# Kernel optimization log

Measured on AMD Instinct MI355X. Metric: run time of the kernel, lower is better.

## Reference

```python
import jax, jax.numpy as jnp
import numpy as np

# Dimensions (see shape_source)
N, M, C = 64, 300, 768          # batch, tokens (=max_frames), token dim
LAMB, G, K = 2, 8, 64           # expansion, groups, clusters
GS = LAMB * C // G              # group_size = 192
DESC = K * GS                   # 12288 NeXtVLAD descriptor dim
NB, NCLS = 512, 701             # bottleneck, classes


def setup_inputs() -> dict:
    key = jax.random.key(0)
    ks = jax.random.split(key, 8)
    w = lambda i, shape: jax.random.normal(ks[i], shape, jnp.float32) * 0.02
    return {
        "features": jax.random.normal(ks[0], (N, M + 1, C), jnp.float32),
        # NeXtVLAD_block params
        "fc0_w": w(1, (LAMB * C, C)), "fc0_b": jnp.zeros((LAMB * C,), jnp.float32),
        "fcgk_w": w(2, (G * K, LAMB * C)), "fcgk_b": jnp.zeros((G * K,), jnp.float32),
        "fcg_w": w(3, (G, LAMB * C)), "fcg_b": jnp.zeros((G,), jnp.float32),
        "bn0_g": jnp.ones((M,), jnp.float32), "bn0_b": jnp.zeros((M,), jnp.float32),
        "cw2": jax.random.uniform(ks[4], (1, GS, K), jnp.float32),
        "bn1_g": jnp.ones((1,), jnp.float32), "bn1_b": jnp.zeros((1,), jnp.float32),
        # ClassBlock params (Linear -> BN -> Linear classifier)
        "cls_fc_w": w(5, (NB, DESC)), "cls_fc_b": jnp.zeros((NB,), jnp.float32),
        "cls_bn_g": jnp.ones((NB,), jnp.float32), "cls_bn_b": jnp.zeros((NB,), jnp.float32),
        "cls_w": w(6, (NCLS, NB)), "cls_b": jnp.zeros((NCLS,), jnp.float32),
    }


def reference(features, fc0_w, fc0_b, fcgk_w, fcgk_b, fcg_w, fcg_b,
              bn0_g, bn0_b, cw2, bn1_g, bn1_b,
              cls_fc_w, cls_fc_b, cls_bn_g, cls_bn_b, cls_w, cls_b):
    # Drop CLS token -> local descriptors (N, M, C). (transpose+vector2image
    # in the torch code is a pure rearrangement back to (N, M, C) tokens.)
    x = features[:, 1:]
    # 1) expand D -> lamb*D
    x_dot = jnp.einsum('nmc,ec->nme', x, fc0_w) + fc0_b           # (N, M, lamb*C)
    # 2) group: (N, M*G, group_size)
    x_tilde = x_dot.reshape(-1, M * G, GS)
    # 3) soft assignment logits, BN over the frame axis (inference-mode BN:
    #    running stats 0/1 -> pure per-frame affine), softmax over clusters
    WgkX = jnp.einsum('nme,fe->nmf', x_dot, fcgk_w) + fcgk_b      # (N, M, G*K)
    WgkX = WgkX * bn0_g[None, :, None] + bn0_b[None, :, None]
    alpha_gk = jax.nn.softmax(WgkX.reshape(-1, M * G, K), axis=-1)
    # 4) sigmoid group attention
    alpha_g = jax.nn.sigmoid(jnp.einsum('nme,ge->nmg', x_dot, fcg_w) + fcg_b)
    alpha_g = alpha_g.reshape(-1, M * G, 1)
    activation = alpha_gk * alpha_g                                # (N, M*G, K)
    # 5) aggregate residuals: vlad = act^T x_tilde - a_sum * centers
    a = jnp.sum(activation, axis=1, keepdims=True) * cw2           # (N, GS, K)
    vlad = jnp.einsum('npk,npd->ndk', activation, x_tilde) - a     # (N, GS, K)
    # 6) L1-normalize over group_size dim (F.normalize(vlad, 1): p=1, dim=1)
    norm = jnp.maximum(jnp.sum(jnp.abs(vlad), axis=1, keepdims=True), 1e-12)
    vlad = (vlad / norm).reshape(-1, DESC)
    # bn1 = BatchNorm1d(1), inference mode -> scalar affine
    vlad = vlad * bn1_g[0] + bn1_b[0]
    # ClassBlock: Linear -> BN (inference affine) -> classifier Linear
    f = jnp.einsum('nd,bd->nb', vlad, cls_fc_w) + cls_fc_b         # (N, NB)
    f = f * cls_bn_g + cls_bn_b
    cls = jnp.einsum('nb,cb->nc', f, cls_w) + cls_b                # (N, NCLS)
    return (cls, f)
```

## Files before the change

### kernel.cpp

```cpp
#include <hip/hip_runtime.h>
#include <hip/hip_bf16.h>

#define NN 64
#define MM 300
#define CC 768
#define EE 1536
#define GG 8
#define KK 64
#define FF 512
#define GS 192
#define PP 2400
#define DESC 12288
#define NMROWS 19200
#define NB 512
#define NCLS 701

typedef _Float16 v8h __attribute__((ext_vector_type(8)));
typedef _Float16 v4h __attribute__((ext_vector_type(4)));
typedef float    v4f __attribute__((ext_vector_type(4)));

#define GLOAD_LDS16(g, s) \
    __builtin_amdgcn_global_load_lds( \
        (const __attribute__((address_space(1))) void*)(g), \
        (__attribute__((address_space(3))) void*)(s), 16, 0, 0)

__global__ __launch_bounds__(256)
void setup_k(const float* __restrict__ features, const float* __restrict__ fc0_w,
             const float* __restrict__ fcgk_w, const float* __restrict__ fcg_w,
             const float* __restrict__ fc0_b, const float* __restrict__ fcgk_b,
             const float* __restrict__ fcg_b,
             _Float16* __restrict__ xf16, _Float16* __restrict__ w1f16,
             _Float16* __restrict__ w2f16, _Float16* __restrict__ w1t16,
             float* __restrict__ biasc, float* __restrict__ wgc)
{
    __shared__ __align__(16) char sm[16640];
    const int bid = blockIdx.x, tid = threadIdx.x;

    if (bid < 14400) {
        int idx = bid * 256 + tid;
        int row = idx / 192;
        int c4  = (idx - row * 192) * 4;
        int n = row / 300, m = row - n * 300;
        float4 v = *(const float4*)(features + ((size_t)(n * 301 + m + 1)) * CC + c4);
        v4h h = { (_Float16)v.x, (_Float16)v.y, (_Float16)v.z, (_Float16)v.w };
        *(v4h*)(xf16 + (size_t)row * CC + c4) = h;
        return;
    }
    if (bid < 15552) {
        int idx = (bid - 14400) * 256 + tid;
        float4 v = *(const float4*)(fc0_w + (size_t)idx * 4);
        v4h h = { (_Float16)v.x, (_Float16)v.y, (_Float16)v.z, (_Float16)v.w };
        *(v4h*)(w1f16 + (size_t)idx * 4) = h;
        return;
    }
    if (bid < 16320) {
        int idx = (bid - 15552) * 256 + tid;
        float4 v = *(const float4*)(fcgk_w + (size_t)idx * 4);
        v4h h = { (_Float16)v.x, (_Float16)v.y, (_Float16)v.z, (_Float16)v.w };
        *(v4h*)(w2f16 + (size_t)idx * 4) = h;
        return;
    }
    if (bid < 16608) {
        float (*T)[65] = (float(*)[65])sm;
        int b = bid - 16320;
        const int c0 = (b % 12) * 64, e0 = (b / 12) * 64;
        const int tc = tid & 63, te = tid >> 6;
        #pragma unroll
        for (int r = 0; r < 16; ++r) {
            int el = te * 16 + r;
            T[el][tc] = fc0_w[(size_t)(e0 + el) * CC + c0 + tc];
        }
        __syncthreads();
        #pragma unroll
        for (int r = 0; r < 16; ++r) {
            int cl = te * 16 + r;
            w1t16[(size_t)(c0 + cl) * EE + e0 + tc] = (_Float16)T[tc][cl];
        }
        return;
    }
    if (bid < 17128) {
        float* red = (float*)sm;
        int f = bid - 16608;
        const float* row = (f < FF) ? (fcgk_w + (size_t)f * EE)
                                    : (fcg_w + (size_t)(f - FF) * EE);
        float s = 0.f;
        for (int e = tid; e < EE; e += 256) s += row[e] * fc0_b[e];
        red[tid] = s;
        __syncthreads();
        for (int o = 128; o; o >>= 1) {
            if (tid < o) red[tid] += red[tid + o];
            __syncthreads();
        }
        if (tid == 0)
            biasc[f] = red[0] + ((f < FF) ? fcgk_b[f] : fcg_b[f - FF]);
        return;
    }
    {
        float (*red)[GG][64] = (float(*)[GG][64])sm;
        int b = bid - 17128;
        const int c = (b % 12) * 64 + (tid & 63);
        const int es = b / 12, q = tid >> 6;
        float acc[GG] = {};
        for (int e = es * 192 + q * 48; e < es * 192 + q * 48 + 48; ++e) {
            float w1v = fc0_w[(size_t)e * CC + c];
            #pragma unroll
            for (int g = 0; g < GG; ++g) acc[g] = fmaf(fcg_w[g * EE + e], w1v, acc[g]);
        }
        #pragma unroll
        for (int g = 0; g < GG; ++g) red[q][g][tid & 63] = acc[g];
        __syncthreads();
        if (tid < 64) {
            #pragma unroll
            for (int g = 0; g < GG; ++g) {
                float v = red[0][g][tid] + red[1][g][tid] + red[2][g][tid] + red[3][g][tid];
                atomicAdd(&wgc[g * CC + c], v);
            }
        }
        return;
    }
}

template<bool OUTF16, bool BN0, bool SOFTGATE, bool BIAS>
__global__ __launch_bounds__(256)
void hgemm_nt(const _Float16* __restrict__ A, const _Float16* __restrict__ B,
              const float* __restrict__ bias,
              const float* __restrict__ bn_g, const float* __restrict__ bn_b,
              const float* __restrict__ sig,
              void* __restrict__ Cout, int Ndim, int Kdim, int gx)
{
    __shared__ __align__(16) _Float16 As[128 * 32];
    __shared__ __align__(16) _Float16 Bs[128 * 32];

    const int tid  = threadIdx.x;
    const int bid  = blockIdx.x;
    const int wave = tid >> 6, lane = tid & 63;
    const int bx = bid % gx, by = bid / gx;
    const int wr = wave >> 1, wc = wave & 1;
    const int row0 = by * 128, col0 = bx * 128;

    const int r0 = tid >> 2, cs = tid & 3;
    const int cc = cs ^ ((r0 >> 1) & 3);
    const _Float16* ga0 = A + (size_t)(row0 + r0) * Kdim + cc * 8;
    const _Float16* ga1 = A + (size_t)(row0 + r0 + 64) * Kdim + cc * 8;
    const _Float16* gb0 = B + (size_t)(col0 + r0) * Kdim + cc * 8;
    const _Float16* gb1 = B + (size_t)(col0 + r0 + 64) * Kdim + cc * 8;
    _Float16* sa0 = As + wave * 512;
    _Float16* sa1 = As + 2048 + wave * 512;
    _Float16* sb0 = Bs + wave * 512;
    _Float16* sb1 = Bs + 2048 + wave * 512;

    v4f acc[4][4];
    #pragma unroll
    for (int i = 0; i < 4; ++i)
        #pragma unroll
        for (int j = 0; j < 4; ++j)
            acc[i][j] = (v4f){0.f, 0.f, 0.f, 0.f};

    const int fm = lane & 15, fq = lane >> 4;
    const int sw = (fm >> 1) & 3;
    const _Float16* arp = As + (wr * 64 + fm) * 32 + (fq ^ sw) * 8;
    const _Float16* brp = Bs + (wc * 64 + fm) * 32 + (fq ^ sw) * 8;

    for (int kt = 0; kt < Kdim; kt += 32) {
        GLOAD_LDS16(ga0 + kt, sa0);
        GLOAD_LDS16(ga1 + kt, sa1);
        GLOAD_LDS16(gb0 + kt, sb0);
        GLOAD_LDS16(gb1 + kt, sb1);
        __syncthreads();

        v8h af[4], bf[4];
        #pragma unroll
        for (int i = 0; i < 4; ++i) af[i] = *(const v8h*)(arp + i * 16 * 32);
        #pragma unroll
        for (int j = 0; j < 4; ++j) bf[j] = *(const v8h*)(brp + j * 16 * 32);
        #pragma unroll
        for (int i = 0; i < 4; ++i)
            #pragma unroll
            for (int j = 0; j < 4; ++j)
                acc[i][j] = __builtin_amdgcn_mfma_f32_16x16x32_f16(
                    af[i], bf[j], acc[i][j], 0, 0, 0);
        __syncthreads();
    }

    float bj[4];
    #pragma unroll
    for (int j = 0; j < 4; ++j)
        bj[j] = BIAS ? bias[col0 + wc * 64 + j * 16 + fm] : 0.f;

    if (SOFTGATE) {
        const int gidx = (col0 >> 6) + wc;
        #pragma unroll
        for (int i = 0; i < 4; ++i) {
            #pragma unroll
            for (int r = 0; r < 4; ++r) {
                int grow = row0 + wr * 64 + i * 16 + fq * 4 + r;
                int n = grow / 300, mm = grow - n * 300;
                float g = bn_g[mm], bb = bn_b[mm];
                float v[4];
                #pragma unroll
                for (int j = 0; j < 4; ++j)
                    v[j] = (acc[i][j][r] + bj[j]) * g + bb;
                float mx = fmaxf(fmaxf(v[0], v[1]), fmaxf(v[2], v[3]));
                #pragma unroll
                for (int w = 1; w < 16; w <<= 1) mx = fmaxf(mx, __shfl_xor(mx, w));
                float e[4], s = 0.f;
                #pragma unroll
                for (int j = 0; j < 4; ++j) { e[j] = __expf(v[j] - mx); s += e[j]; }
                #pragma unroll
                for (int w = 1; w < 16; w <<= 1) s += __shfl_xor(s, w);
                float gate = sig[(size_t)grow * GG + gidx];
                float inv = gate / s;
                _Float16* cp = (_Float16*)Cout + (size_t)grow * Ndim + col0 + wc * 64;
                #pragma unroll
                for (int j = 0; j < 4; ++j) cp[j * 16 + fm] = (_Float16)(e[j] * inv);
            }
        }
        return;
    }

    #pragma unroll
    for (int i = 0; i < 4; ++i) {
        #pragma unroll
        for (int r = 0; r < 4; ++r) {
            int grow = row0 + wr * 64 + i * 16 + fq * 4 + r;
            float g = 1.f, bb = 0.f;
            if (BN0) { int m = grow % 300; g = bn_g[m]; bb = bn_b[m]; }
            #pragma unroll
            for (int j = 0; j < 4; ++j) {
                int gcol = col0 + wc * 64 + j * 16 + fm;
                float v = acc[i][j][r] + bj[j];
                if (BN0) v = v * g + bb;
                if (OUTF16)
                    ((_Float16*)Cout)[(size_t)grow * Ndim + gcol] = (_Float16)v;
                else
                    ((float*)Cout)[(size_t)grow * Ndim + gcol] = v;
            }
        }
    }
}

__global__ __launch_bounds__(256)
void alpha_sig_k(const _Float16* __restrict__ x, const float* __restrict__ wgc,
                 const float* __restrict__ bgc, float* __restrict__ sig)
{
    __shared__ float W[GG * CC];
    for (int i = threadIdx.x; i < GG * CC; i += 256) W[i] = wgc[i];
    __syncthreads();

    const int wave = threadIdx.x >> 6;
    const int lane = threadIdx.x & 63;

    for (int rr = 0; rr < 4; ++rr) {
        int row = blockIdx.x * 16 + wave * 4 + rr;
        const _Float16* xr = x + (size_t)row * CC;
        float acc[GG] = {};
        for (int c = lane; c < CC; c += 64) {
            float xv = (float)xr[c];
            #pragma unroll
            for (int g = 0; g < GG; ++g) acc[g] = fmaf(xv, W[g * CC + c], acc[g]);
        }
        float myval = 0.f;
        #pragma unroll
        for (int g = 0; g < GG; ++g) {
            float s = acc[g];
            #pragma unroll
            for (int o = 32; o; o >>= 1) s += __shfl_xor(s, o);
            if (lane == g) myval = s + bgc[g];
        }
        if (lane < GG)
            sig[(size_t)row * GG + lane] = 1.f / (1.f + __expf(-myval));
    }
}

__global__ __launch_bounds__(256)
void vladact_k(const _Float16* __restrict__ act, const _Float16* __restrict__ xdot,
               float* __restrict__ part, float* __restrict__ apart)
{
    __shared__ __align__(16) char sm[8192];
    const int tid = threadIdx.x, bid = blockIdx.x;

    if (bid >= 1536) {
        float (*red)[64] = (float(*)[64])sm;
        int b = bid - 1536;
        const int ps = b & 7, n = b >> 3;
        const int k = tid & 63, q = tid >> 6;
        const _Float16* base = act + ((size_t)n * PP + ps * 300 + q * 75) * 64 + k;
        float s = 0.f;
        for (int p = 0; p < 75; ++p) s += (float)base[(size_t)p * 64];
        red[q][k] = s;
        __syncthreads();
        if (tid < 64)
            apart[((size_t)ps * NN + n) * 64 + tid] =
                red[0][tid] + red[1][tid] + red[2][tid] + red[3][tid];
        return;
    }

    float (*As)[64] = (float(*)[64])sm;
    float (*Xs)[64] = (float(*)[64])(sm + 4096);
    const int dt = bid % 3, n = (bid / 3) & 63, ps = bid / 192;
    const int d0 = dt * 64;
    const int p0 = ps * 300, pend = p0 + 300;
    const int tx = tid & 15, ty = tid >> 4;
    const int kb = tx * 4, db = ty * 4;
    const _Float16* actn = act + (size_t)n * PP * 64;
    const _Float16* xn   = xdot + (size_t)n * MM * EE;
    float acc[4][4] = {};

    const int lpp = tid >> 4, lk4 = (tid & 15) << 2;
    for (int pc = p0; pc < pend; pc += 16) {
        int p = pc + lpp;
        float a0 = 0.f, a1 = 0.f, a2 = 0.f, a3 = 0.f;
        float x0 = 0.f, x1 = 0.f, x2 = 0.f, x3 = 0.f;
        if (p < pend) {
            v4h avh = *(const v4h*)(actn + (size_t)p * 64 + lk4);
            a0 = (float)avh[0]; a1 = (float)avh[1]; a2 = (float)avh[2]; a3 = (float)avh[3];
            v4h xv = *(const v4h*)(xn + (size_t)(p >> 3) * EE + (p & 7) * GS + d0 + lk4);
            x0 = (float)xv[0]; x1 = (float)xv[1]; x2 = (float)xv[2]; x3 = (float)xv[3];
        }
        As[lpp][lk4 + 0] = a0; As[lpp][lk4 + 1] = a1;
        As[lpp][lk4 + 2] = a2; As[lpp][lk4 + 3] = a3;
        Xs[lpp][lk4 + 0] = x0; Xs[lpp][lk4 + 1] = x1;
        Xs[lpp][lk4 + 2] = x2; Xs[lpp][lk4 + 3] = x3;
        __syncthreads();
        #pragma unroll
        for (int q = 0; q < 16; ++q) {
            float4 a4 = *(const float4*)&As[q][kb];
            float4 x4 = *(const float4*)&Xs[q][db];
            float aa[4] = {a4.x, a4.y, a4.z, a4.w};
            float xx[4] = {x4.x, x4.y, x4.z, x4.w};
            #pragma unroll
            for (int i = 0; i < 4; ++i)
                #pragma unroll
                for (int j = 0; j < 4; ++j)
                    acc[i][j] = fmaf(xx[i], aa[j], acc[i][j]);
        }
        __syncthreads();
    }

    float* pp = part + ((size_t)ps * NN + n) * DESC;
    #pragma unroll
    for (int i = 0; i < 4; ++i) {
        int dd = d0 + db + i;
        float4 o = {acc[i][0], acc[i][1], acc[i][2], acc[i][3]};
        *(float4*)(pp + (size_t)dd * 64 + kb) = o;
    }
}

__global__ __launch_bounds__(256)
void vladnorm_k(const float* __restrict__ part, const float* __restrict__ apart,
                const float* __restrict__ cw2, const float* __restrict__ bn1g,
                const float* __restrict__ bn1b, float* __restrict__ vlad)
{
    const int n = blockIdx.x >> 2, kq = blockIdx.x & 3;
    const int tk = threadIdx.x & 15, td = threadIdx.x >> 4;
    const int k = kq * 16 + tk;

    float a = 0.f;
    #pragma unroll
    for (int ps = 0; ps < 8; ++ps) a += apart[((size_t)ps * NN + n) * 64 + k];

    float vloc[12];
    float sabs = 0.f;
    #pragma unroll
    for (int i = 0; i < 12; ++i) {
        int d = td * 12 + i;
        float s = 0.f;
        #pragma unroll
        for (int ps = 0; ps < 8; ++ps)
            s += part[((size_t)ps * NN + n) * DESC + (size_t)d * 64 + k];
        float v = s - a * cw2[d * 64 + k];
        vloc[i] = v;
        sabs += fabsf(v);
    }

    __shared__ float red[16][16];
    __shared__ float inv[16];
    red[td][tk] = sabs;
    __syncthreads();
    if (td == 0) {
        float t = 0.f;
        #pragma unroll
        for (int q = 0; q < 16; ++q) t += red[q][tk];
        inv[tk] = 1.f / fmaxf(t, 1e-12f);
    }
    __syncthreads();
    const float g = bn1g[0], b = bn1b[0];
    const float sc = inv[tk] * g;
    #pragma unroll
    for (int i = 0; i < 12; ++i) {
        int d = td * 12 + i;
        vlad[(size_t)n * DESC + (size_t)d * 64 + k] = vloc[i] * sc + b;
    }
}

__global__ __launch_bounds__(256)
void fsplit_k(const float* __restrict__ vlad, const float* __restrict__ W,
              float* __restrict__ part)
{
    const int bcol0 = (blockIdx.x & 7) * 64;
    const int ks = blockIdx.x >> 3;
    const int kc0 = ks * 256;
    __shared__ float Vs[32][68];
    __shared__ float Ws[32][68];
    const int tid = threadIdx.x, tx = tid & 15, ty = tid >> 4;
    float acc[4][4] = {};

    for (int kc = kc0; kc < kc0 + 256; kc += 32) {
        #pragma unroll
        for (int it = 0; it < 2; ++it) {
            int sl = tid + it * 256;
            int rr = sl >> 3, k4 = (sl & 7) << 2;
            float4 v = *(const float4*)(vlad + (size_t)rr * DESC + kc + k4);
            Vs[k4+0][rr] = v.x; Vs[k4+1][rr] = v.y; Vs[k4+2][rr] = v.z; Vs[k4+3][rr] = v.w;
            float4 w = *(const float4*)(W + (size_t)(bcol0 + rr) * DESC + kc + k4);
            Ws[k4+0][rr] = w.x; Ws[k4+1][rr] = w.y; Ws[k4+2][rr] = w.z; Ws[k4+3][rr] = w.w;
        }
        __syncthreads();
        #pragma unroll
        for (int q = 0; q < 32; ++q) {
            float4 wv = *(const float4*)&Ws[q][tx*4];
            float4 vv = *(const float4*)&Vs[q][ty*4];
            float wa[4] = {wv.x, wv.y, wv.z, wv.w};
            float va[4] = {vv.x, vv.y, vv.z, vv.w};
            #pragma unroll
            for (int i = 0; i < 4; ++i)
                #pragma unroll
                for (int j = 0; j < 4; ++j)
                    acc[i][j] = fmaf(va[i], wa[j], acc[i][j]);
        }
        __syncthreads();
    }
    float* p = part + (size_t)ks * (NN * NB);
    #pragma unroll
    for (int i = 0; i < 4; ++i) {
        int n = ty * 4 + i;
        float4 o = {acc[i][0], acc[i][1], acc[i][2], acc[i][3]};
        *(float4*)(p + (size_t)n * NB + bcol0 + tx*4) = o;
    }
}

__global__ __launch_bounds__(256)
void freduce_k(const float* __restrict__ part, const float* __restrict__ bias,
               const float* __restrict__ bng, const float* __restrict__ bnb,
               float* __restrict__ f)
{
    int idx = blockIdx.x * 256 + threadIdx.x;
    float s = 0.f;
    for (int ks = 0; ks < 48; ++ks) s += part[(size_t)ks * (NN * NB) + idx];
    int b = idx & (NB - 1);
    f[idx] = (s + bias[b]) * bng[b] + bnb[b];
}

__global__ __launch_bounds__(256)
void cls_k(const float* __restrict__ f, const float* __restrict__ W,
           const float* __restrict__ bias, float* __restrict__ out)
{
    const int c0 = (blockIdx.x % 11) * 64;
    const int ks = blockIdx.x / 11;
    __shared__ float Fs[32][68];
    __shared__ float Ws[32][68];
    const int tid = threadIdx.x, tx = tid & 15, ty = tid >> 4;
    float acc[4][4] = {};

    for (int kc = ks * 128; kc < ks * 128 + 128; kc += 32) {
        #pragma unroll
        for (int it = 0; it < 2; ++it) {
            int sl = tid + it * 256;
            int rr = sl >> 3, k4 = (sl & 7) << 2;
            float4 v = *(const float4*)(f + (size_t)rr * NB + kc + k4);
            Fs[k4+0][rr] = v.x; Fs[k4+1][rr] = v.y; Fs[k4+2][rr] = v.z; Fs[k4+3][rr] = v.w;
            int c = c0 + rr;
            float4 w = (c < NCLS) ? *(const float4*)(W + (size_t)c * NB + kc + k4)
                                  : make_float4(0.f, 0.f, 0.f, 0.f);
            Ws[k4+0][rr] = w.x; Ws[k4+1][rr] = w.y; Ws[k4+2][rr] = w.z; Ws[k4+3][rr] = w.w;
        }
        __syncthreads();
        #pragma unroll
        for (int q = 0; q < 32; ++q) {
            float4 wv = *(const float4*)&Ws[q][tx*4];
            float4 fv = *(const float4*)&Fs[q][ty*4];
            float wa[4] = {wv.x, wv.y, wv.z, wv.w};
            float fa[4] = {fv.x, fv.y, fv.z, fv.w};
            #pragma unroll
            for (int i = 0; i < 4; ++i)
                #pragma unroll
                for (int j = 0; j < 4; ++j)
                    acc[i][j] = fmaf(fa[i], wa[j], acc[i][j]);
        }
        __syncthreads();
    }
    #pragma unroll
    for (int i = 0; i < 4; ++i) {
        int n = ty * 4 + i;
        #pragma unroll
        for (int j = 0; j < 4; ++j) {
            int c = c0 + tx * 4 + j;
            if (c < NCLS) {
                float v = acc[i][j] + ((ks == 0) ? bias[c] : 0.f);
                atomicAdd(&out[(size_t)n * NCLS + c], v);
            }
        }
    }
}

extern "C" void kernel_launch(void* const* d_in, const int* in_sizes, int n_in,
                              void* d_out, int out_size, void* d_ws, size_t ws_size,
                              hipStream_t stream)
{
    const float* features = (const float*)d_in[0];
    const float* fc0_w    = (const float*)d_in[1];
    const float* fc0_b    = (const float*)d_in[2];
    const float* fcgk_w   = (const float*)d_in[3];
    const float* fcgk_b   = (const float*)d_in[4];
    const float* fcg_w    = (const float*)d_in[5];
    const float* fcg_b    = (const float*)d_in[6];
    const float* bn0_g    = (const float*)d_in[7];
    const float* bn0_b    = (const float*)d_in[8];
    const float* cw2      = (const float*)d_in[9];
    const float* bn1_g    = (const float*)d_in[10];
    const float* bn1_b    = (const float*)d_in[11];
    const float* cls_fc_w = (const float*)d_in[12];
    const float* cls_fc_b = (const float*)d_in[13];
    const float* cls_bn_g = (const float*)d_in[14];
    const float* cls_bn_b = (const float*)d_in[15];
    const float* cls_w    = (const float*)d_in[16];
    const float* cls_b    = (const float*)d_in[17];

    char* ws = (char*)d_ws;
    _Float16* xf16   = (_Float16*)(ws + 0);
    _Float16* w1f16  = (_Float16*)(ws + 29491200);
    _Float16* w2f16  = (_Float16*)(ws + 31850496);
    _Float16* w1t16  = (_Float16*)(ws + 33423360);
    _Float16* w2cf16 = (_Float16*)(ws + 35782656);
    float*    biasc  = (float*)   (ws + 36569088);
    float*    wgc    = (float*)   (ws + 36573184);
    _Float16* xdot16 = (_Float16*)(ws + 36597760);
    _Float16* act16  = (_Float16*)(ws + 95580160);
    float*    sigma  = (float*)   (ws + 115240960);
    float*    apart  = (float*)   (ws + 115855360);
    float*    vpart  = (float*)   (ws + 115986432);
    float*    vlad   = (float*)   (ws + 141152256);
    float*    fpart  = (float*)   (ws + 144297984);

    float* cls_out = (float*)d_out;
    float* f_out   = cls_out + NN * NCLS;

    dim3 blk(256);

    hipMemsetAsync(wgc, 0, GG * CC * sizeof(float), stream);
    hipMemsetAsync(cls_out, 0, (size_t)NN * NCLS * sizeof(float), stream);

    setup_k<<<17224, blk, 0, stream>>>(features, fc0_w, fcgk_w, fcg_w,
                                       fc0_b, fcgk_b, fcg_b,
                                       xf16, w1f16, w2f16, w1t16, biasc, wgc);

    hgemm_nt<true, false, false, false><<<24, blk, 0, stream>>>(
        w2f16, w1t16, nullptr, nullptr, nullptr, nullptr, w2cf16, CC, EE, 6);

    hgemm_nt<true, false, false, true><<<1800, blk, 0, stream>>>(
        xf16, w1f16, fc0_b, nullptr, nullptr, nullptr, xdot16, EE, CC, 12);

    alpha_sig_k<<<1200, blk, 0, stream>>>(xf16, wgc, biasc + FF, sigma);

    hgemm_nt<true, true, true, true><<<600, blk, 0, stream>>>(
        xf16, w2cf16, biasc, bn0_g, bn0_b, sigma, act16, FF, CC, 4);

    vladact_k<<<2048, blk, 0, stream>>>(act16, xdot16, vpart, apart);

    vladnorm_k<<<256, blk, 0, stream>>>(vpart, apart, cw2, bn1_g, bn1_b, vlad);

    fsplit_k<<<384, blk, 0, stream>>>(vlad, cls_fc_w, fpart);
    freduce_k<<<128, blk, 0, stream>>>(fpart, cls_fc_b, cls_bn_g, cls_bn_b, f_out);

    cls_k<<<44, blk, 0, stream>>>(f_out, cls_w, cls_b, cls_out);
}
```

Measured before the change: 448.6 us.

## Fuse sigmoid gate into softmax GEMM, merge GEMM launches, drop memsets and reduce kernel

The group-sigmoid attention is computed inside the soft-assignment GEMM main loop from the A fragments already staged in shared memory, which removes the separate alpha_sig kernel and its sigma buffer. The small weight-combining GEMM is folded into the x_dot GEMM launch as extra blocks. The memsets move into setup_k, and wgc is written directly instead of accumulated with atomics. The fsplit partials are atomically added into f with the BN affine applied, which removes freduce_k, and cls_k now runs without split-K atomics. These changes cut launches and intermediate traffic, at the cost of extra FMAs in the GEMM loop and nondeterministic atomic summation order.

```diff
diff --git a/kernel.cpp b/kernel.cpp
--- a/kernel.cpp
+++ b/kernel.cpp
@@ -14,6 +14,7 @@
 #define NMROWS 19200
 #define NB 512
 #define NCLS 701
+#define OUTSZ (NN*NCLS + NN*NB)
 
 typedef _Float16 v8h __attribute__((ext_vector_type(8)));
 typedef _Float16 v4h __attribute__((ext_vector_type(4)));
@@ -31,7 +32,8 @@
              const float* __restrict__ fcg_b,
              _Float16* __restrict__ xf16, _Float16* __restrict__ w1f16,
              _Float16* __restrict__ w2f16, _Float16* __restrict__ w1t16,
-             float* __restrict__ biasc, float* __restrict__ wgc)
+             float* __restrict__ biasc, float* __restrict__ wgc,
+             float* __restrict__ dout)
 {
     __shared__ __align__(16) char sm[16640];
     const int bid = blockIdx.x, tid = threadIdx.x;
@@ -95,13 +97,13 @@
             biasc[f] = red[0] + ((f < FF) ? fcgk_b[f] : fcg_b[f - FF]);
         return;
     }
-    {
+    if (bid < 17140) {
         float (*red)[GG][64] = (float(*)[GG][64])sm;
         int b = bid - 17128;
-        const int c = (b % 12) * 64 + (tid & 63);
-        const int es = b / 12, q = tid >> 6;
+        const int c = b * 64 + (tid & 63);
+        const int q = tid >> 6;
         float acc[GG] = {};
-        for (int e = es * 192 + q * 48; e < es * 192 + q * 48 + 48; ++e) {
+        for (int e = q * 384; e < q * 384 + 384; ++e) {
             float w1v = fc0_w[(size_t)e * CC + c];
             #pragma unroll
             for (int g = 0; g < GG; ++g) acc[g] = fmaf(fcg_w[g * EE + e], w1v, acc[g]);
@@ -111,39 +113,57 @@
         __syncthreads();
         if (tid < 64) {
             #pragma unroll
-            for (int g = 0; g < GG; ++g) {
-                float v = red[0][g][tid] + red[1][g][tid] + red[2][g][tid] + red[3][g][tid];
-                atomicAdd(&wgc[g * CC + c], v);
-            }
-        }
-        return;
-    }
-}
-
-template<bool OUTF16, bool BN0, bool SOFTGATE, bool BIAS>
+            for (int g = 0; g < GG; ++g)
+                wgc[g * CC + c] = red[0][g][tid] + red[1][g][tid]
+                                + red[2][g][tid] + red[3][g][tid];
+        }
+        return;
+    }
+    {
+        int b = bid - 17140;
+        for (int idx = b * 256 + tid; idx < OUTSZ; idx += 10 * 256)
+            dout[idx] = 0.f;
+        return;
+    }
+}
+
+template<bool OUTF16, bool BN0, bool SOFTGATE>
 __global__ __launch_bounds__(256)
 void hgemm_nt(const _Float16* __restrict__ A, const _Float16* __restrict__ B,
               const float* __restrict__ bias,
               const float* __restrict__ bn_g, const float* __restrict__ bn_b,
-              const float* __restrict__ sig,
-              void* __restrict__ Cout, int Ndim, int Kdim, int gx)
+              const float* __restrict__ wgc, const float* __restrict__ gbias,
+              void* __restrict__ Cout, int Ndim, int Kdim, int gx,
+              int nblk1,
+              const _Float16* __restrict__ A2, const _Float16* __restrict__ B2,
+              void* __restrict__ C2, int Ndim2, int Kdim2, int gx2)
 {
     __shared__ __align__(16) _Float16 As[128 * 32];
     __shared__ __align__(16) _Float16 Bs[128 * 32];
+    __shared__ float gsm[4][64];
 
     const int tid  = threadIdx.x;
-    const int bid  = blockIdx.x;
+    int bid = blockIdx.x;
+    const _Float16* Ap = A; const _Float16* Bp = B; void* Cp = Cout;
+    const float* bp = bias;
+    int Nd = Ndim, Kd = Kdim, g = gx;
+    if (bid >= nblk1) {
+        bid -= nblk1;
+        Ap = A2; Bp = B2; Cp = C2; Nd = Ndim2; Kd = Kdim2; g = gx2;
+        bp = nullptr;
+    }
+
     const int wave = tid >> 6, lane = tid & 63;
-    const int bx = bid % gx, by = bid / gx;
+    const int bx = bid % g, by = bid / g;
     const int wr = wave >> 1, wc = wave & 1;
     const int row0 = by * 128, col0 = bx * 128;
 
     const int r0 = tid >> 2, cs = tid & 3;
     const int cc = cs ^ ((r0 >> 1) & 3);
-    const _Float16* ga0 = A + (size_t)(row0 + r0) * Kdim + cc * 8;
-    const _Float16* ga1 = A + (size_t)(row0 + r0 + 64) * Kdim + cc * 8;
-    const _Float16* gb0 = B + (size_t)(col0 + r0) * Kdim + cc * 8;
-    const _Float16* gb1 = B + (size_t)(col0 + r0 + 64) * Kdim + cc * 8;
+    const _Float16* ga0 = Ap + (size_t)(row0 + r0) * Kd + cc * 8;
+    const _Float16* ga1 = Ap + (size_t)(row0 + r0 + 64) * Kd + cc * 8;
+    const _Float16* gb0 = Bp + (size_t)(col0 + r0) * Kd + cc * 8;
+    const _Float16* gb1 = Bp + (size_t)(col0 + r0 + 64) * Kd + cc * 8;
     _Float16* sa0 = As + wave * 512;
     _Float16* sa1 = As + 2048 + wave * 512;
     _Float16* sb0 = Bs + wave * 512;
@@ -161,7 +181,11 @@
     const _Float16* arp = As + (wr * 64 + fm) * 32 + (fq ^ sw) * 8;
     const _Float16* brp = Bs + (wc * 64 + fm) * 32 + (fq ^ sw) * 8;
 
-    for (int kt = 0; kt < Kdim; kt += 32) {
+    const int gidx = SOFTGATE ? ((col0 >> 6) + wc) : 0;
+    const float* wg = SOFTGATE ? (wgc + (size_t)gidx * CC) : nullptr;
+    float gacc[4] = {0.f, 0.f, 0.f, 0.f};
+
+    for (int kt = 0; kt < Kd; kt += 32) {
         GLOAD_LDS16(ga0 + kt, sa0);
         GLOAD_LDS16(ga1 + kt, sa1);
         GLOAD_LDS16(gb0 + kt, sb0);
@@ -173,6 +197,18 @@
         for (int i = 0; i < 4; ++i) af[i] = *(const v8h*)(arp + i * 16 * 32);
         #pragma unroll
         for (int j = 0; j < 4; ++j) bf[j] = *(const v8h*)(brp + j * 16 * 32);
+
+        if (SOFTGATE) {
+            float4 wv0 = *(const float4*)(wg + kt + fq * 8);
+            float4 wv1 = *(const float4*)(wg + kt + fq * 8 + 4);
+            float w8[8] = {wv0.x, wv0.y, wv0.z, wv0.w, wv1.x, wv1.y, wv1.z, wv1.w};
+            #pragma unroll
+            for (int i = 0; i < 4; ++i)
+                #pragma unroll
+                for (int j = 0; j < 8; ++j)
+                    gacc[i] = fmaf((float)af[i][j], w8[j], gacc[i]);
+        }
+
         #pragma unroll
         for (int i = 0; i < 4; ++i)
             #pragma unroll
@@ -185,21 +221,29 @@
     float bj[4];
     #pragma unroll
     for (int j = 0; j < 4; ++j)
-        bj[j] = BIAS ? bias[col0 + wc * 64 + j * 16 + fm] : 0.f;
+        bj[j] = bp ? bp[col0 + wc * 64 + j * 16 + fm] : 0.f;
 
     if (SOFTGATE) {
-        const int gidx = (col0 >> 6) + wc;
+        const float gb = gbias[gidx];
         #pragma unroll
         for (int i = 0; i < 4; ++i) {
+            float s = gacc[i];
+            s += __shfl_xor(s, 16);
+            s += __shfl_xor(s, 32);
+            gsm[wave][i * 16 + fm] = 1.f / (1.f + __expf(-(s + gb)));
+        }
+        #pragma unroll
+        for (int i = 0; i < 4; ++i) {
             #pragma unroll
             for (int r = 0; r < 4; ++r) {
-                int grow = row0 + wr * 64 + i * 16 + fq * 4 + r;
+                int lrow = i * 16 + fq * 4 + r;
+                int grow = row0 + wr * 64 + lrow;
                 int n = grow / 300, mm = grow - n * 300;
-                float g = bn_g[mm], bb = bn_b[mm];
+                float gsc = bn_g[mm], bb = bn_b[mm];
                 float v[4];
                 #pragma unroll
                 for (int j = 0; j < 4; ++j)
-                    v[j] = (acc[i][j][r] + bj[j]) * g + bb;
+                    v[j] = (acc[i][j][r] + bj[j]) * gsc + bb;
                 float mx = fmaxf(fmaxf(v[0], v[1]), fmaxf(v[2], v[3]));
                 #pragma unroll
                 for (int w = 1; w < 16; w <<= 1) mx = fmaxf(mx, __shfl_xor(mx, w));
@@ -208,9 +252,9 @@
                 for (int j = 0; j < 4; ++j) { e[j] = __expf(v[j] - mx); s += e[j]; }
                 #pragma unroll
                 for (int w = 1; w < 16; w <<= 1) s += __shfl_xor(s, w);
-                float gate = sig[(size_t)grow * GG + gidx];
+                float gate = gsm[wave][lrow];
                 float inv = gate / s;
-                _Float16* cp = (_Float16*)Cout + (size_t)grow * Ndim + col0 + wc * 64;
+                _Float16* cp = (_Float16*)Cp + (size_t)grow * Nd + col0 + wc * 64;
                 #pragma unroll
                 for (int j = 0; j < 4; ++j) cp[j * 16 + fm] = (_Float16)(e[j] * inv);
             }
@@ -223,52 +267,19 @@
         #pragma unroll
         for (int r = 0; r < 4; ++r) {
             int grow = row0 + wr * 64 + i * 16 + fq * 4 + r;
-            float g = 1.f, bb = 0.f;
-            if (BN0) { int m = grow % 300; g = bn_g[m]; bb = bn_b[m]; }
+            float gsc = 1.f, bb = 0.f;
+            if (BN0) { int m = grow % 300; gsc = bn_g[m]; bb = bn_b[m]; }
             #pragma unroll
             for (int j = 0; j < 4; ++j) {
                 int gcol = col0 + wc * 64 + j * 16 + fm;
                 float v = acc[i][j][r] + bj[j];
-                if (BN0) v = v * g + bb;
+                if (BN0) v = v * gsc + bb;
                 if (OUTF16)
-                    ((_Float16*)Cout)[(size_t)grow * Ndim + gcol] = (_Float16)v;
+                    ((_Float16*)Cp)[(size_t)grow * Nd + gcol] = (_Float16)v;
                 else
-                    ((float*)Cout)[(size_t)grow * Ndim + gcol] = v;
+                    ((float*)Cp)[(size_t)grow * Nd + gcol] = v;
             }
         }
-    }
-}
-
-__global__ __launch_bounds__(256)
-void alpha_sig_k(const _Float16* __restrict__ x, const float* __restrict__ wgc,
-                 const float* __restrict__ bgc, float* __restrict__ sig)
-{
-    __shared__ float W[GG * CC];
-    for (int i = threadIdx.x; i < GG * CC; i += 256) W[i] = wgc[i];
-    __syncthreads();
-
-    const int wave = threadIdx.x >> 6;
-    const int lane = threadIdx.x & 63;
-
-    for (int rr = 0; rr < 4; ++rr) {
-        int row = blockIdx.x * 16 + wave * 4 + rr;
-        const _Float16* xr = x + (size_t)row * CC;
-        float acc[GG] = {};
-        for (int c = lane; c < CC; c += 64) {
-            float xv = (float)xr[c];
-            #pragma unroll
-            for (int g = 0; g < GG; ++g) acc[g] = fmaf(xv, W[g * CC + c], acc[g]);
-        }
-        float myval = 0.f;
-        #pragma unroll
-        for (int g = 0; g < GG; ++g) {
-            float s = acc[g];
-            #pragma unroll
-            for (int o = 32; o; o >>= 1) s += __shfl_xor(s, o);
-            if (lane == g) myval = s + bgc[g];
-        }
-        if (lane < GG)
-            sig[(size_t)row * GG + lane] = 1.f / (1.f + __expf(-myval));
     }
 }
 
@@ -395,7 +406,8 @@
 
 __global__ __launch_bounds__(256)
 void fsplit_k(const float* __restrict__ vlad, const float* __restrict__ W,
-              float* __restrict__ part)
+              const float* __restrict__ bias, const float* __restrict__ bng,
+              const float* __restrict__ bnb, float* __restrict__ f)
 {
     const int bcol0 = (blockIdx.x & 7) * 64;
     const int ks = blockIdx.x >> 3;
@@ -430,39 +442,36 @@
         }
         __syncthreads();
     }
-    float* p = part + (size_t)ks * (NN * NB);
+
+    float gj[4], cj[4];
+    #pragma unroll
+    for (int j = 0; j < 4; ++j) {
+        int b = bcol0 + tx * 4 + j;
+        gj[j] = bng[b];
+        cj[j] = (ks == 0) ? (bias[b] * bng[b] + bnb[b]) : 0.f;
+    }
     #pragma unroll
     for (int i = 0; i < 4; ++i) {
         int n = ty * 4 + i;
-        float4 o = {acc[i][0], acc[i][1], acc[i][2], acc[i][3]};
-        *(float4*)(p + (size_t)n * NB + bcol0 + tx*4) = o;
-    }
-}
-
-__global__ __launch_bounds__(256)
-void freduce_k(const float* __restrict__ part, const float* __restrict__ bias,
-               const float* __restrict__ bng, const float* __restrict__ bnb,
-               float* __restrict__ f)
-{
-    int idx = blockIdx.x * 256 + threadIdx.x;
-    float s = 0.f;
-    for (int ks = 0; ks < 48; ++ks) s += part[(size_t)ks * (NN * NB) + idx];
-    int b = idx & (NB - 1);
-    f[idx] = (s + bias[b]) * bng[b] + bnb[b];
+        #pragma unroll
+        for (int j = 0; j < 4; ++j) {
+            int b = bcol0 + tx * 4 + j;
+            atomicAdd(&f[(size_t)n * NB + b], acc[i][j] * gj[j] + cj[j]);
+        }
+    }
 }
 
 __global__ __launch_bounds__(256)
 void cls_k(const float* __restrict__ f, const float* __restrict__ W,
            const float* __restrict__ bias, float* __restrict__ out)
 {
-    const int c0 = (blockIdx.x % 11) * 64;
-    const int ks = blockIdx.x / 11;
+    const int c0 = blockIdx.x * 64;
     __shared__ float Fs[32][68];
     __shared__ float Ws[32][68];
     const int tid = threadIdx.x, tx = tid & 15, ty = tid >> 4;
     float acc[4][4] = {};
 
-    for (int kc = ks * 128; kc < ks * 128 + 128; kc += 32) {
+    for (int kc = 0; kc < NB; kc += 32) {
         #pragma unroll
         for (int it = 0; it < 2; ++it) {
             int sl = tid + it * 256;
@@ -495,10 +504,7 @@
         #pragma unroll
         for (int j = 0; j < 4; ++j) {
             int c = c0 + tx * 4 + j;
-            if (c < NCLS) {
-                float v = acc[i][j] + ((ks == 0) ? bias[c] : 0.f);
-                atomicAdd(&out[(size_t)n * NCLS + c], v);
-            }
+            if (c < NCLS) out[(size_t)n * NCLS + c] = acc[i][j] + bias[c];
         }
     }
 }
@@ -536,41 +542,36 @@
     float*    wgc    = (float*)   (ws + 36573184);
     _Float16* xdot16 = (_Float16*)(ws + 36597760);
     _Float16* act16  = (_Float16*)(ws + 95580160);
-    float*    sigma  = (float*)   (ws + 115240960);
-    float*    apart  = (float*)   (ws + 115855360);
-    float*    vpart  = (float*)   (ws + 115986432);
-    float*    vlad   = (float*)   (ws + 141152256);
-    float*    fpart  = (float*)   (ws + 144297984);
+    float*    apart  = (float*)   (ws + 115240960);
+    float*    vpart  = (float*)   (ws + 115372032);
+    float*    vlad   = (float*)   (ws + 140537856);
 
     float* cls_out = (float*)d_out;
     float* f_out   = cls_out + NN * NCLS;
 
     dim3 blk(256);
 
-    hipMemsetAsync(wgc, 0, GG * CC * sizeof(float), stream);
-    hipMemsetAsync(cls_out, 0, (size_t)NN * NCLS * sizeof(float), stream);
-
-    setup_k<<<17224, blk, 0, stream>>>(features, fc0_w, fcgk_w, fcg_w,
+    setup_k<<<17150, blk, 0, stream>>>(features, fc0_w, fcgk_w, fcg_w,
                                        fc0_b, fcgk_b, fcg_b,
-                                       xf16, w1f16, w2f16, w1t16, biasc, wgc);
-
-    hgemm_nt<true, false, false, false><<<24, blk, 0, stream>>>(
-        w2f16, w1t16, nullptr, nullptr, nullptr, nullptr, w2cf16, CC, EE, 6);
-
-    hgemm_nt<true, false, false, true><<<1800, blk, 0, stream>>>(
-        xf16, w1f16, fc0_b, nullptr, nullptr, nullptr, xdot16, EE, CC, 12);
-
-    alpha_sig_k<<<1200, blk, 0, stream>>>(xf16, wgc, biasc + FF, sigma);
-
-    hgemm_nt<true, true, true, true><<<600, blk, 0, stream>>>(
-        xf16, w2cf16, biasc, bn0_g, bn0_b, sigma, act16, FF, CC, 4);
+                                       xf16, w1f16, w2f16, w1t16, biasc, wgc,
+                                       (float*)d_out);
+
+    hgemm_nt<true, false, false><<<1824, blk, 0, stream>>>(
+        xf16, w1f16, fc0_b, nullptr, nullptr, nullptr, nullptr,
+        xdot16, EE, CC, 12,
+        1800, w2f16, w1t16, w2cf16, CC, EE, 6);
+
+    hgemm_nt<true, true, true><<<600, blk, 0, stream>>>(
+        xf16, w2cf16, biasc, bn0_g, bn0_b, wgc, biasc + FF,
+        act16, FF, CC, 4,
+        600, nullptr, nullptr, nullptr, 0, 0, 1);
 
     vladact_k<<<2048, blk, 0, stream>>>(act16, xdot16, vpart, apart);
 
     vladnorm_k<<<256, blk, 0, stream>>>(vpart, apart, cw2, bn1_g, bn1_b, vlad);
 
-    fsplit_k<<<384, blk, 0, stream>>>(vlad, cls_fc_w, fpart);
-    freduce_k<<<128, blk, 0, stream>>>(fpart, cls_fc_b, cls_bn_g, cls_bn_b, f_out);
-
-    cls_k<<<44, blk, 0, stream>>>(f_out, cls_w, cls_b, cls_out);
-}
+    fsplit_k<<<384, blk, 0, stream>>>(vlad, cls_fc_w, cls_fc_b,
+                                      cls_bn_g, cls_bn_b, f_out);
+
+    cls_k<<<11, blk, 0, stream>>>(f_out, cls_w, cls_b, cls_out);
+}
```

After: 474.7 us. 1.06x slower.
